# Kernel tuning notes

Hardware: AMD Instinct MI355X
Metric: run time of the kernel (lower is better)

Reference implementation:

```python
import jax, jax.numpy as jnp
import numpy as np

B, S, E = 4, 1024, 1024
H, DH = 16, 64
P = 64  # prompt length
MASKED_BIAS = -10000.0


def setup_inputs() -> dict:
    key = jax.random.key(0)
    ks = jax.random.split(key, 9)
    return {
        "hidden_states": jax.random.normal(ks[0], (B, S, E), jnp.float32),
        "promptKey": jax.random.normal(ks[1], (B, H, P, DH), jnp.float32),
        "promptValue": jax.random.normal(ks[2], (B, H, P, DH), jnp.float32),
        "textualKey": jax.random.normal(ks[3], (B, H, S, DH), jnp.float32),
        "textualValue": jax.random.normal(ks[4], (B, H, S, DH), jnp.float32),
        "promptMask": jnp.ones((B, 1, S, P), jnp.bool_),
        "c_attn_w": jax.random.normal(ks[5], (E, 3 * E), jnp.float32) * 0.02,
        "c_attn_b": jnp.zeros((3 * E,), jnp.float32),
        "c_proj_w": jax.random.normal(ks[6], (E, E), jnp.float32) * 0.02,
        "c_proj_b": jnp.zeros((E,), jnp.float32),
    }


def _split_heads(t):
    # [B, S, E] -> [B, H, S, DH]
    b, s, _ = t.shape
    return t.reshape(b, s, H, DH).transpose(0, 2, 1, 3)


def reference(hidden_states, promptKey, promptValue, textualKey, textualValue,
              promptMask, c_attn_w, c_attn_b, c_proj_w, c_proj_b):
    qkv = hidden_states @ c_attn_w + c_attn_b          # [B,S,3E]
    q, k, v = jnp.split(qkv, 3, axis=-1)
    q, k, v = _split_heads(q), _split_heads(k), _split_heads(v)  # [B,H,S,DH]

    # scores against prompt KV, textual KV, and elementwise self term
    promptW = jnp.einsum("bhsd,bhpd->bhsp", q, promptKey)       # [B,H,S,P]
    textW = jnp.einsum("bhsd,bhtd->bhst", q, textualKey)        # [B,H,S,S]
    selfW = jnp.sum(q * k, axis=-1, keepdims=True)              # [B,H,S,1]
    attn_weights = jnp.concatenate((promptW, textW, selfW), axis=-1)
    attn_weights = attn_weights / jnp.sqrt(jnp.float32(DH))

    # non-residual causal mask: bias[qlen-qlen:qlen, 1:klen+1] -> strictly lower tri
    causal = jnp.tri(S, S, -1, dtype=bool)                      # [S,S]
    self_mask = jnp.ones((S, 1), dtype=bool)
    causal_self = jnp.concatenate((causal, self_mask), axis=-1)[None, None]  # [1,1,S,S+1]
    full_mask = jnp.concatenate(
        (promptMask, jnp.broadcast_to(causal_self, (B, 1, S, S + 1))), axis=-1)
    attn_weights = jnp.where(full_mask, attn_weights, MASKED_BIAS)
    attn_weights = jax.nn.softmax(attn_weights, axis=-1)

    wSelf = attn_weights[..., -1:]                              # [B,H,S,1]
    wRest = attn_weights[..., :-1]                              # [B,H,S,P+S]
    valuePast = jnp.concatenate((promptValue, textualValue), axis=-2)  # [B,H,P+S,DH]
    attn_output = jnp.einsum("bhsk,bhkd->bhsd", wRest, valuePast) + wSelf * v

    # merge heads and output projection
    attn_output = attn_output.transpose(0, 2, 1, 3).reshape(B, S, E)
    return attn_output @ c_proj_w + c_proj_b
```

## Files before the change

kernel.cpp:

```cpp
#include <hip/hip_runtime.h>
#include <hip/hip_bf16.h>
#include <stdint.h>

#define H_ 16
#define DH_ 64
#define S_ 1024
#define B_ 4
#define E_ 1024
#define P_ 64
#define BH_ (B_ * H_)
#define KV_ (P_ + S_)
#define NT_ 17
#define TILE_ELEMS 4096

typedef __attribute__((ext_vector_type(8))) short short8;
typedef __attribute__((ext_vector_type(4))) float floatx4;

#define MFMA_BF16(a, b, c) __builtin_amdgcn_mfma_f32_16x16x32_bf16((a), (b), (c), 0, 0, 0)

__device__ __forceinline__ float bf2f(unsigned short u) {
    union { float f; uint32_t i; } x;
    x.i = ((uint32_t)u) << 16;
    return x.f;
}
__device__ __forceinline__ unsigned short f2bf(float f) {
    uint32_t i = __float_as_uint(f);
    uint32_t r = (i + 0x7fffu + ((i >> 16) & 1u)) >> 16;
    return (unsigned short)r;
}

__device__ __forceinline__ void gl_lds16(const void* g, void* l) {
    __builtin_amdgcn_global_load_lds(
        (const __attribute__((address_space(1))) uint32_t*)g,
        (__attribute__((address_space(3))) uint32_t*)l, 16, 0, 0);
}

#define BARRIER() asm volatile("s_barrier" ::: "memory")
#define WAIT_VM(n) asm volatile("s_waitcnt vmcnt(" #n ")" ::: "memory")

__global__ void prep(const float* __restrict__ hidden, const float* __restrict__ cw,
                     const float* __restrict__ pw, const float* __restrict__ pK,
                     const float* __restrict__ tK, const float* __restrict__ pV,
                     const float* __restrict__ tV, unsigned short* __restrict__ Ah,
                     unsigned short* __restrict__ Wt1, unsigned short* __restrict__ Wt2,
                     unsigned short* __restrict__ Kp, unsigned short* __restrict__ Vp) {
    __shared__ float t[32][33];
    int bid = blockIdx.x, tid = threadIdx.x;
    if (bid < 4096) {
        int i = bid * 256 + tid;
        float4 v = ((const float4*)hidden)[i];
        ushort4 o;
        o.x = f2bf(v.x); o.y = f2bf(v.y); o.z = f2bf(v.z); o.w = f2bf(v.w);
        ((ushort4*)Ah)[i] = o;
    } else if (bid < 8192) {
        const float* in; unsigned short* out; int R, C, bxx, byy;
        if (bid < 7168) { int i = bid - 4096; in = cw; out = Wt1; R = 1024; C = 3072; bxx = i % 96; byy = i / 96; }
        else            { int i = bid - 7168; in = pw; out = Wt2; R = 1024; C = 1024; bxx = i % 32; byy = i / 32; }
        int tx = tid & 31, ty = tid >> 5;
        int c0 = bxx * 32, r0 = byy * 32;
#pragma unroll
        for (int i = 0; i < 4; ++i)
            t[ty + i * 8][tx] = in[(size_t)(r0 + ty + i * 8) * C + c0 + tx];
        __syncthreads();
#pragma unroll
        for (int i = 0; i < 4; ++i)
            out[(size_t)(c0 + ty + i * 8) * R + r0 + tx] = f2bf(t[tx][ty + i * 8]);
    } else {
        int gid0 = (bid - 8192) * 256 + tid;
        int half = gid0 / (BH_ * 8704);
        int gid = gid0 % (BH_ * 8704);
        int bh = gid / 8704, rem = gid % 8704;
        int tt = rem / 512, r2 = rem % 512;
        int f = r2 >> 6, lane = r2 & 63;
        int nt = f >> 1, h = f & 1, quad = lane >> 4, cl = lane & 15;
        unsigned short o[8];
        if (half == 0) {
            int key = tt * 64 + nt * 16 + cl;
            int dh = h * 32 + quad * 8;
            const float* src = (key < P_)
                ? pK + ((size_t)bh * P_ + key) * DH_ + dh
                : tK + ((size_t)bh * S_ + (key - P_)) * DH_ + dh;
#pragma unroll
            for (int u = 0; u < 8; ++u) o[u] = f2bf(src[u]);
            *(int4*)&Kp[(size_t)gid * 8] = *(int4*)o;
        } else {
            int dhn = nt * 16 + cl;
            int kbase = tt * 64 + h * 32 + quad * 8;
            const float* src = (kbase < P_)
                ? pV + ((size_t)bh * P_ + kbase) * DH_ + dhn
                : tV + ((size_t)bh * S_ + (kbase - P_)) * DH_ + dhn;
#pragma unroll
            for (int u = 0; u < 8; ++u) o[u] = f2bf(src[(size_t)u * DH_]);
            *(int4*)&Vp[(size_t)gid * 8] = *(int4*)o;
        }
    }
}

template <int MODE, int TM, int TN, int BK>
__global__ __launch_bounds__(256) void gemm_bt(
    const unsigned short* __restrict__ A, const unsigned short* __restrict__ Bt,
    const float* __restrict__ bias, float* __restrict__ Cout,
    unsigned short* __restrict__ Qo, unsigned short* __restrict__ Ko,
    unsigned short* __restrict__ Vo, int M, int N, int K) {
    constexpr int MI = TM / 32, NI = TN / 32;
    constexpr int NA = TM * BK / 2048;
    constexpr int NB = TN * BK / 2048;
    static_assert(NA + NB == 4, "vmcnt constant assumes 4 loads/tile");
    __shared__ __align__(16) unsigned short lA[2][TM * BK];
    __shared__ __align__(16) unsigned short lB[2][TN * BK];
    int tid = threadIdx.x;
    int wave = tid >> 6, lane = tid & 63, quad = lane >> 4, cl = lane & 15;
    int m0 = blockIdx.y * TM, n0 = blockIdx.x * TN;
    int wm = (wave >> 1) * (TM / 2), wn = (wave & 1) * (TN / 2);
    floatx4 acc[MI][NI];
#pragma unroll
    for (int mi = 0; mi < MI; ++mi)
#pragma unroll
        for (int ni = 0; ni < NI; ++ni) acc[mi][ni] = (floatx4){0.f, 0.f, 0.f, 0.f};

    auto issue = [&](int k0, int buf) {
#pragma unroll
        for (int li = 0; li < NA; ++li) {
            int o = (li * 256 + tid) * 16;
            int hh = o / (TM * 64), rr = (o % (TM * 64)) >> 6, c8 = (o >> 4) & 3;
            gl_lds16(A + (size_t)(m0 + rr) * K + k0 + hh * 32 + c8 * 8,
                     (char*)lA[buf] + o);
        }
#pragma unroll
        for (int li = 0; li < NB; ++li) {
            int o = (li * 256 + tid) * 16;
            int hh = o / (TN * 64), rr = (o % (TN * 64)) >> 6, c8 = (o >> 4) & 3;
            gl_lds16(Bt + (size_t)(n0 + rr) * K + k0 + hh * 32 + c8 * 8,
                     (char*)lB[buf] + o);
        }
    };
    auto compute = [&](int buf) {
#pragma unroll
        for (int kk = 0; kk < BK / 32; ++kk) {
            short8 af[MI], bfr[NI];
#pragma unroll
            for (int mi = 0; mi < MI; ++mi)
                af[mi] = *(const short8*)&lA[buf][kk * TM * 32 + (wm + mi * 16 + cl) * 32 + quad * 8];
#pragma unroll
            for (int ni = 0; ni < NI; ++ni)
                bfr[ni] = *(const short8*)&lB[buf][kk * TN * 32 + (wn + ni * 16 + cl) * 32 + quad * 8];
#pragma unroll
            for (int mi = 0; mi < MI; ++mi)
#pragma unroll
                for (int ni = 0; ni < NI; ++ni)
                    acc[mi][ni] = MFMA_BF16(af[mi], bfr[ni], acc[mi][ni]);
        }
    };

    int nT = K / BK;
    issue(0, 0);
    for (int t = 0; t < nT; ++t) {
        int buf = t & 1;
        if (t + 1 < nT) {
            issue((t + 1) * BK, buf ^ 1);
            WAIT_VM(4);
        } else {
            WAIT_VM(0);
        }
        BARRIER();
        compute(buf);
        BARRIER();
    }

#pragma unroll
    for (int ni = 0; ni < NI; ++ni) {
        int ncol = n0 + wn + ni * 16 + cl;
        float bv = bias[ncol];
#pragma unroll
        for (int mi = 0; mi < MI; ++mi) {
#pragma unroll
            for (int r = 0; r < 4; ++r) {
                int mrow = m0 + wm + mi * 16 + quad * 4 + r;
                float v = acc[mi][ni][r] + bv;
                if (MODE == 0) {
                    Cout[(size_t)mrow * N + ncol] = v;
                } else {
                    int which = ncol >> 10, e = ncol & 1023;
                    int hh = e >> 6, dh = e & 63;
                    int b = mrow >> 10, s = mrow & 1023;
                    size_t idx = ((size_t)(b * H_ + hh) * S_ + s) * DH_ + dh;
                    unsigned short* dst = (which == 0) ? Qo : ((which == 1) ? Ko : Vo);
                    dst[idx] = f2bf(v);
                }
            }
        }
    }
}

__global__ __launch_bounds__(256) void attn_k(
    const unsigned short* __restrict__ Q, const unsigned short* __restrict__ Kc,
    const unsigned short* __restrict__ Vc, const unsigned short* __restrict__ Kp,
    const unsigned short* __restrict__ Vp, unsigned short* __restrict__ Aout) {
    __shared__ __align__(16) unsigned short lK[TILE_ELEMS];
    __shared__ __align__(16) unsigned short lV[TILE_ELEMS];
    __shared__ __align__(16) unsigned short lP[4][16 * 72];
    int tid = threadIdx.x, wave = tid >> 6, lane = tid & 63;
    int quad = lane >> 4, cl = lane & 15;
    int p = blockIdx.x, bh = blockIdx.y;
    int b = bh >> 4, h = bh & 15;
    const unsigned short* Qb = Q + (size_t)bh * S_ * DH_;
    const unsigned short* Kb = Kc + (size_t)bh * S_ * DH_;
    const unsigned short* Vb = Vc + (size_t)bh * S_ * DH_;
    const unsigned short* Kpb = Kp + (size_t)bh * NT_ * TILE_ELEMS;
    const unsigned short* Vpb = Vp + (size_t)bh * NT_ * TILE_ELEMS;
    unsigned short* lp = lP[wave];
    int so = wave * 1024 + lane * 16;

    for (int seg = 0; seg < 2; ++seg) {
        int x = seg ? (15 - p) : p;
        int qb = x * 64 + wave * 16;

        short8 a0 = *(const short8*)(Qb + (size_t)(qb + cl) * DH_ + quad * 8);
        short8 a1 = *(const short8*)(Qb + (size_t)(qb + cl) * DH_ + quad * 8 + 32);

        float lsum[4] = {0.f, 0.f, 0.f, 0.f};
        floatx4 O[4];
#pragma unroll
        for (int nt = 0; nt < 4; ++nt) O[nt] = (floatx4){0.f, 0.f, 0.f, 0.f};

        int T = x + 2;
        for (int t = 0; t < T; ++t) {
            __syncthreads();
            {
                const char* gK = (const char*)(Kpb + (size_t)t * TILE_ELEMS);
                const char* gV = (const char*)(Vpb + (size_t)t * TILE_ELEMS);
                gl_lds16(gK + so, (char*)lK + so);
                gl_lds16(gK + 4096 + so, (char*)lK + 4096 + so);
                gl_lds16(gV + so, (char*)lV + so);
                gl_lds16(gV + 4096 + so, (char*)lV + 4096 + so);
            }
            __syncthreads();

            floatx4 s[4];
#pragma unroll
            for (int nt = 0; nt < 4; ++nt) {
                s[nt] = (floatx4){0.f, 0.f, 0.f, 0.f};
                short8 k0 = *(const short8*)&lK[(nt * 2 + 0) * 512 + lane * 8];
                short8 k1 = *(const short8*)&lK[(nt * 2 + 1) * 512 + lane * 8];
                s[nt] = MFMA_BF16(a0, k0, s[nt]);
                s[nt] = MFMA_BF16(a1, k1, s[nt]);
            }
            bool diag = (t == T - 1);
            int rl = wave * 16 + quad * 4;
#pragma unroll
            for (int nt = 0; nt < 4; ++nt) {
                int col = nt * 16 + cl;
#pragma unroll
                for (int r = 0; r < 4; ++r) {
                    float v = s[nt][r] * 0.125f;
                    if (diag && col >= rl + r) v = -10000.0f;
                    float pb = __expf(v);
                    lsum[r] += pb;
                    lp[(quad * 4 + r) * 72 + col] = f2bf(pb);
                }
            }
            asm volatile("s_waitcnt lgkmcnt(0)" ::: "memory");
            short8 p0 = *(const short8*)&lp[cl * 72 + quad * 8];
            short8 p1 = *(const short8*)&lp[cl * 72 + quad * 8 + 32];
#pragma unroll
            for (int nt = 0; nt < 4; ++nt) {
                short8 v0 = *(const short8*)&lV[(nt * 2 + 0) * 512 + lane * 8];
                short8 v1 = *(const short8*)&lV[(nt * 2 + 1) * 512 + lane * 8];
                O[nt] = MFMA_BF16(p0, v0, O[nt]);
                O[nt] = MFMA_BF16(p1, v1, O[nt]);
            }
        }

#pragma unroll
        for (int r = 0; r < 4; ++r) {
            float rs = lsum[r];
            rs += __shfl_xor(rs, 1, 16);
            rs += __shfl_xor(rs, 2, 16);
            rs += __shfl_xor(rs, 4, 16);
            rs += __shfl_xor(rs, 8, 16);
            int row = qb + quad * 4 + r;
            const unsigned short* qp = Qb + (size_t)row * DH_ + cl * 4;
            const unsigned short* kp = Kb + (size_t)row * DH_ + cl * 4;
            float d = 0.f;
#pragma unroll
            for (int u = 0; u < 4; ++u) d += bf2f(qp[u]) * bf2f(kp[u]);
            d += __shfl_xor(d, 1, 16);
            d += __shfl_xor(d, 2, 16);
            d += __shfl_xor(d, 4, 16);
            d += __shfl_xor(d, 8, 16);
            float ps = __expf(d * 0.125f);
            float linv = 1.0f / (rs + ps);
#pragma unroll
            for (int nt = 0; nt < 4; ++nt) {
                float vv = bf2f(Vb[(size_t)row * DH_ + nt * 16 + cl]);
                float o = (O[nt][r] + ps * vv) * linv;
                Aout[((size_t)b * S_ + row) * E_ + h * DH_ + nt * 16 + cl] = f2bf(o);
            }
        }
    }
}

extern "C" void kernel_launch(void* const* d_in, const int* in_sizes, int n_in,
                              void* d_out, int out_size, void* d_ws, size_t ws_size,
                              hipStream_t stream) {
    const float* hidden = (const float*)d_in[0];
    const float* pK = (const float*)d_in[1];
    const float* pV = (const float*)d_in[2];
    const float* tK = (const float*)d_in[3];
    const float* tV = (const float*)d_in[4];
    const float* cw = (const float*)d_in[6];
    const float* cb = (const float*)d_in[7];
    const float* pw = (const float*)d_in[8];
    const float* pb = (const float*)d_in[9];
    float* out = (float*)d_out;

    unsigned short* ws = (unsigned short*)d_ws;
    unsigned short* Wt1 = ws;
    unsigned short* Wt2 = Wt1 + (size_t)3072 * 1024;
    unsigned short* Ah  = Wt2 + (size_t)1024 * 1024;
    unsigned short* Qw  = Ah + (size_t)4096 * 1024;
    unsigned short* Kw  = Qw + (size_t)BH_ * S_ * DH_;
    unsigned short* Vw  = Kw + (size_t)BH_ * S_ * DH_;
    unsigned short* Kp  = Vw + (size_t)BH_ * S_ * DH_;
    unsigned short* Vp  = Kp + (size_t)BH_ * NT_ * TILE_ELEMS;
    unsigned short* At  = Ah;

    prep<<<12544, 256, 0, stream>>>(hidden, cw, pw, pK, tK, pV, tV,
                                    Ah, Wt1, Wt2, Kp, Vp);
    gemm_bt<1, 128, 128, 32><<<dim3(3072 / 128, 4096 / 128), 256, 0, stream>>>(
        Ah, Wt1, cb, nullptr, Qw, Kw, Vw, 4096, 3072, 1024);
    attn_k<<<dim3(8, BH_), 256, 0, stream>>>(Qw, Kw, Vw, Kp, Vp, At);
    gemm_bt<0, 64, 64, 64><<<dim3(1024 / 64, 4096 / 128 * 2), 256, 0, stream>>>(
        At, Wt2, pb, out, nullptr, nullptr, nullptr, 4096, 1024, 1024);
}
```

Baseline: 210.9 us.

## Share KV tile loads between paired query blocks in attention kernel

```diff
diff --git a/kernel.cpp b/kernel.cpp
--- a/kernel.cpp
+++ b/kernel.cpp
@@ -201,7 +201,8 @@
     __shared__ __align__(16) unsigned short lP[4][16 * 72];
     int tid = threadIdx.x, wave = tid >> 6, lane = tid & 63;
     int quad = lane >> 4, cl = lane & 15;
-    int p = blockIdx.x, bh = blockIdx.y;
+    int l = blockIdx.x;
+    int p = l >> 6, bh = l & 63;
     int b = bh >> 4, h = bh & 15;
     const unsigned short* Qb = Q + (size_t)bh * S_ * DH_;
     const unsigned short* Kb = Kc + (size_t)bh * S_ * DH_;
@@ -211,66 +212,80 @@
     unsigned short* lp = lP[wave];
     int so = wave * 1024 + lane * 16;
 
+    int x1 = p, x2 = 15 - p;
+    int qb1 = x1 * 64 + wave * 16, qb2 = x2 * 64 + wave * 16;
+
+    short8 a0_1 = *(const short8*)(Qb + (size_t)(qb1 + cl) * DH_ + quad * 8);
+    short8 a1_1 = *(const short8*)(Qb + (size_t)(qb1 + cl) * DH_ + quad * 8 + 32);
+    short8 a0_2 = *(const short8*)(Qb + (size_t)(qb2 + cl) * DH_ + quad * 8);
+    short8 a1_2 = *(const short8*)(Qb + (size_t)(qb2 + cl) * DH_ + quad * 8 + 32);
+
+    float lsum1[4] = {0.f, 0.f, 0.f, 0.f}, lsum2[4] = {0.f, 0.f, 0.f, 0.f};
+    floatx4 O1[4], O2[4];
+#pragma unroll
+    for (int nt = 0; nt < 4; ++nt) {
+        O1[nt] = (floatx4){0.f, 0.f, 0.f, 0.f};
+        O2[nt] = (floatx4){0.f, 0.f, 0.f, 0.f};
+    }
+
+    int rl = wave * 16 + quad * 4;
+
+    auto do_tile = [&](short8 a0, short8 a1, floatx4* O, float* lsum, bool diag) {
+        floatx4 s[4];
+#pragma unroll
+        for (int nt = 0; nt < 4; ++nt) {
+            s[nt] = (floatx4){0.f, 0.f, 0.f, 0.f};
+            short8 k0 = *(const short8*)&lK[(nt * 2 + 0) * 512 + lane * 8];
+            short8 k1 = *(const short8*)&lK[(nt * 2 + 1) * 512 + lane * 8];
+            s[nt] = MFMA_BF16(a0, k0, s[nt]);
+            s[nt] = MFMA_BF16(a1, k1, s[nt]);
+        }
+#pragma unroll
+        for (int nt = 0; nt < 4; ++nt) {
+            int col = nt * 16 + cl;
+#pragma unroll
+            for (int r = 0; r < 4; ++r) {
+                float v = s[nt][r] * 0.125f;
+                if (diag && col >= rl + r) v = -10000.0f;
+                float pb = __expf(v);
+                lsum[r] += pb;
+                lp[(quad * 4 + r) * 72 + col] = f2bf(pb);
+            }
+        }
+        asm volatile("s_waitcnt lgkmcnt(0)" ::: "memory");
+        short8 p0 = *(const short8*)&lp[cl * 72 + quad * 8];
+        short8 p1 = *(const short8*)&lp[cl * 72 + quad * 8 + 32];
+#pragma unroll
+        for (int nt = 0; nt < 4; ++nt) {
+            short8 v0 = *(const short8*)&lV[(nt * 2 + 0) * 512 + lane * 8];
+            short8 v1 = *(const short8*)&lV[(nt * 2 + 1) * 512 + lane * 8];
+            O[nt] = MFMA_BF16(p0, v0, O[nt]);
+            O[nt] = MFMA_BF16(p1, v1, O[nt]);
+        }
+    };
+
+    int T1 = x1 + 2, Tu = x2 + 2;
+    for (int t = 0; t < Tu; ++t) {
+        __syncthreads();
+        {
+            const char* gK = (const char*)(Kpb + (size_t)t * TILE_ELEMS);
+            const char* gV = (const char*)(Vpb + (size_t)t * TILE_ELEMS);
+            gl_lds16(gK + so, (char*)lK + so);
+            gl_lds16(gK + 4096 + so, (char*)lK + 4096 + so);
+            gl_lds16(gV + so, (char*)lV + so);
+            gl_lds16(gV + 4096 + so, (char*)lV + 4096 + so);
+        }
+        __syncthreads();
+
+        do_tile(a0_2, a1_2, O2, lsum2, t == Tu - 1);
+        if (t < T1) do_tile(a0_1, a1_1, O1, lsum1, t == T1 - 1);
+    }
+
+#pragma unroll
     for (int seg = 0; seg < 2; ++seg) {
-        int x = seg ? (15 - p) : p;
-        int qb = x * 64 + wave * 16;
-
-        short8 a0 = *(const short8*)(Qb + (size_t)(qb + cl) * DH_ + quad * 8);
-        short8 a1 = *(const short8*)(Qb + (size_t)(qb + cl) * DH_ + quad * 8 + 32);
-
-        float lsum[4] = {0.f, 0.f, 0.f, 0.f};
-        floatx4 O[4];
-#pragma unroll
-        for (int nt = 0; nt < 4; ++nt) O[nt] = (floatx4){0.f, 0.f, 0.f, 0.f};
-
-        int T = x + 2;
-        for (int t = 0; t < T; ++t) {
-            __syncthreads();
-            {
-                const char* gK = (const char*)(Kpb + (size_t)t * TILE_ELEMS);
-                const char* gV = (const char*)(Vpb + (size_t)t * TILE_ELEMS);
-                gl_lds16(gK + so, (char*)lK + so);
-                gl_lds16(gK + 4096 + so, (char*)lK + 4096 + so);
-                gl_lds16(gV + so, (char*)lV + so);
-                gl_lds16(gV + 4096 + so, (char*)lV + 4096 + so);
-            }
-            __syncthreads();
-
-            floatx4 s[4];
-#pragma unroll
-            for (int nt = 0; nt < 4; ++nt) {
-                s[nt] = (floatx4){0.f, 0.f, 0.f, 0.f};
-                short8 k0 = *(const short8*)&lK[(nt * 2 + 0) * 512 + lane * 8];
-                short8 k1 = *(const short8*)&lK[(nt * 2 + 1) * 512 + lane * 8];
-                s[nt] = MFMA_BF16(a0, k0, s[nt]);
-                s[nt] = MFMA_BF16(a1, k1, s[nt]);
-            }
-            bool diag = (t == T - 1);
-            int rl = wave * 16 + quad * 4;
-#pragma unroll
-            for (int nt = 0; nt < 4; ++nt) {
-                int col = nt * 16 + cl;
-#pragma unroll
-                for (int r = 0; r < 4; ++r) {
-                    float v = s[nt][r] * 0.125f;
-                    if (diag && col >= rl + r) v = -10000.0f;
-                    float pb = __expf(v);
-                    lsum[r] += pb;
-                    lp[(quad * 4 + r) * 72 + col] = f2bf(pb);
-                }
-            }
-            asm volatile("s_waitcnt lgkmcnt(0)" ::: "memory");
-            short8 p0 = *(const short8*)&lp[cl * 72 + quad * 8];
-            short8 p1 = *(const short8*)&lp[cl * 72 + quad * 8 + 32];
-#pragma unroll
-            for (int nt = 0; nt < 4; ++nt) {
-                short8 v0 = *(const short8*)&lV[(nt * 2 + 0) * 512 + lane * 8];
-                short8 v1 = *(const short8*)&lV[(nt * 2 + 1) * 512 + lane * 8];
-                O[nt] = MFMA_BF16(p0, v0, O[nt]);
-                O[nt] = MFMA_BF16(p1, v1, O[nt]);
-            }
-        }
-
+        int qb = seg ? qb2 : qb1;
+        float* lsum = seg ? lsum2 : lsum1;
+        floatx4* O = seg ? O2 : O1;
 #pragma unroll
         for (int r = 0; r < 4; ++r) {
             float rs = lsum[r];
@@ -329,7 +344,7 @@
                                     Ah, Wt1, Wt2, Kp, Vp);
     gemm_bt<1, 128, 128, 32><<<dim3(3072 / 128, 4096 / 128), 256, 0, stream>>>(
         Ah, Wt1, cb, nullptr, Qw, Kw, Vw, 4096, 3072, 1024);
-    attn_k<<<dim3(8, BH_), 256, 0, stream>>>(Qw, Kw, Vw, Kp, Vp, At);
+    attn_k<<<512, 256, 0, stream>>>(Qw, Kw, Vw, Kp, Vp, At);
     gemm_bt<0, 64, 64, 64><<<dim3(1024 / 64, 4096 / 128 * 2), 256, 0, stream>>>(
         At, Wt2, pb, out, nullptr, nullptr, nullptr, 4096, 1024, 1024);
 }
```

New measurement: 198.6 us. 5.9% less time.
